# Kernel tuning notes

Hardware: AMD Instinct MI355X
Metric: run time of the kernel (lower is better)

Reference implementation:

```python
import jax, jax.numpy as jnp
import numpy as np

NUM_HEADS = 8
ALPHA = 4.0
BN_EPS = 1e-5


def _dwconv(x, w, pad):
    # x: [B, C, H, W], w: [C, 1, kh, kw] depthwise (groups == C)
    return jax.lax.conv_general_dilated(
        x, w, window_strides=(1, 1), padding=[(pad, pad), (pad, pad)],
        dimension_numbers=('NCHW', 'OIHW', 'NCHW'),
        feature_group_count=x.shape[1])


def _forward(x, qg_w, kv_w, proj_w, proj_b, dwc_w, dwc_b, power_p, scale_p,
             enh_w, bn_gamma, bn_beta, enhance_weight, pos_enc):
    B, N, C = x.shape
    H = W = int(round(N ** 0.5))
    h = NUM_HEADS
    d = C // h

    # qg linear (no bias): [B, N, 2C] -> q, g
    qg = jnp.einsum('bnc,oc->bno', x, qg_w)
    q, g = qg[..., :C], qg[..., C:]

    # SpatialFilterEnhancer on q: depthwise 3x3 conv + BN(train) + ReLU
    qi = q.transpose(0, 2, 1).reshape(B, C, H, W)
    qe = _dwconv(qi, enh_w, pad=1)
    m = qe.mean(axis=(0, 2, 3), keepdims=True)
    var = qe.var(axis=(0, 2, 3), keepdims=True)
    qe = (qe - m) * jax.lax.rsqrt(var + BN_EPS)
    qe = qe * bn_gamma[None, :, None, None] + bn_beta[None, :, None, None]
    qe = jax.nn.relu(qe)
    q_enh = qe.reshape(B, C, N).transpose(0, 2, 1)
    q = q + enhance_weight * q_enh

    # kv linear (sr_ratio == 1 path)
    kv = jnp.einsum('bnc,oc->bno', x, kv_w)
    k, v = kv[..., :C], kv[..., C:]
    k = k + pos_enc  # learned positional encoding, shape [1, N, C]
    n = k.shape[1]

    scale = jax.nn.softplus(scale_p)              # [1, 1, C]
    power = 1.0 + ALPHA * jax.nn.sigmoid(power_p)  # [1, h, 1, d]
    q = q / scale
    k = k / scale

    # split heads: [B, h, N, d]
    q = q.reshape(B, N, h, d).transpose(0, 2, 1, 3)
    k = k.reshape(B, n, h, d).transpose(0, 2, 1, 3)
    v = v.reshape(B, n, h, d).transpose(0, 2, 1, 3)

    # power-law kernel feature maps
    q_pos = jax.nn.relu(q) ** power
    q_neg = jax.nn.relu(-q) ** power
    k_pos = jax.nn.relu(k) ** power
    k_neg = jax.nn.relu(-k) ** power
    q_sim = jnp.concatenate([q_pos, q_neg], axis=-1)   # [B, h, N, 2d]
    q_opp = jnp.concatenate([q_neg, q_pos], axis=-1)
    kf = jnp.concatenate([k_pos, k_neg], axis=-1)      # [B, h, n, 2d]
    v1, v2 = jnp.split(v, 2, axis=-1)                  # [B, h, n, d/2] each

    k_mean = kf.mean(axis=-2)  # [B, h, 2d]
    inv_n = 1.0 / n

    # sim branch
    z = 1.0 / (jnp.einsum('bhnd,bhd->bhn', q_sim, k_mean)[..., None] + 1e-6)
    kv1 = jnp.einsum('bhnd,bhne->bhde', kf, v1) * inv_n  # (n^-0.5)*(n^-0.5)
    x_sim = jnp.einsum('bhnd,bhde->bhne', q_sim, kv1) * z

    # opp branch
    z2 = 1.0 / (jnp.einsum('bhnd,bhd->bhn', q_opp, k_mean)[..., None] + 1e-6)
    kv2 = jnp.einsum('bhnd,bhne->bhde', kf, v2) * inv_n
    x_opp = jnp.einsum('bhnd,bhde->bhne', q_opp, kv2) * z2

    xa = jnp.concatenate([x_sim, x_opp], axis=-1)       # [B, h, N, d]
    xa = xa.transpose(0, 2, 1, 3).reshape(B, N, C)

    # depthwise conv positional branch on v (sr_ratio == 1 -> no interpolate)
    vimg = v.reshape(B * h, H, W, d).transpose(0, 3, 1, 2)  # [B*h, d, H, W]
    vd = _dwconv(vimg, dwc_w, pad=2) + dwc_b[None, :, None, None]
    v_out = vd.reshape(B, C, N).transpose(0, 2, 1)          # [B, N, C]

    out = (xa + v_out) * g
    out = jnp.einsum('bnc,oc->bno', out, proj_w) + proj_b
    return out


def setup_inputs() -> dict:
    key = jax.random.key(0)
    ks = jax.random.split(key, 10)
    B, N, C = 8, 3136, 512
    h = NUM_HEADS
    d = C // h
    f = lambda k, shape, s=0.02: jax.random.normal(k, shape, jnp.float32) * s
    return dict(
        x=jax.random.normal(ks[0], (B, N, C), jnp.float32),
        qg_w=f(ks[1], (2 * C, C)),
        kv_w=f(ks[2], (2 * C, C)),
        proj_w=f(ks[3], (C, C)),
        proj_b=jnp.zeros((C,), jnp.float32),
        dwc_w=f(ks[4], (d, 1, 5, 5), 0.1),
        dwc_b=jnp.zeros((d,), jnp.float32),
        power_p=f(ks[5], (1, h, 1, d), 0.1),
        scale_p=f(ks[6], (1, 1, C), 0.1),
        enh_w=f(ks[7], (C, 1, 3, 3), 0.1),
        bn_gamma=jnp.ones((C,), jnp.float32),
        bn_beta=jnp.zeros((C,), jnp.float32),
        enhance_weight=jnp.float32(0.5),
        pos_enc=f(ks[8], (1, N, C)),
    )


def reference(x, qg_w, kv_w, proj_w, proj_b, dwc_w, dwc_b, power_p, scale_p,
              enh_w, bn_gamma, bn_beta, enhance_weight, pos_enc):
    return _forward(x, qg_w, kv_w, proj_w, proj_b, dwc_w, dwc_b, power_p,
                    scale_p, enh_w, bn_gamma, bn_beta, enhance_weight, pos_enc)
```

## Files before the change

### kernel.cpp

```cpp
#include <hip/hip_runtime.h>
#include <hip/hip_bf16.h>
#include <math.h>

#define CDIM 512
#define NTOK 3136
#define BATCH 8
#define MTOT (BATCH*NTOK)
#define NHEAD 8
#define DHEAD 64
#define HW 56

typedef __attribute__((ext_vector_type(8))) short short8;
typedef __attribute__((ext_vector_type(4))) float f32x4;

__device__ __forceinline__ ushort f2bf(float f) {
    union { float f; unsigned int u; } v; v.f = f;
    unsigned int u = v.u + 0x7FFFu + ((v.u >> 16) & 1u);
    return (ushort)(u >> 16);
}
__device__ __forceinline__ float bf2f(ushort u) {
    union { unsigned int u; float f; } v; v.u = ((unsigned int)u) << 16;
    return v.f;
}

__device__ __forceinline__ void gload_lds16(const void* g, void* lds) {
    __builtin_amdgcn_global_load_lds((const __attribute__((address_space(1))) void*)g,
                                     (__attribute__((address_space(3))) void*)lds,
                                     16, 0, 0);
}

__global__ __launch_bounds__(256) void cvt_bf16_kernel(const float* __restrict__ src,
                                                       ushort* __restrict__ dst, int n4) {
    int i = blockIdx.x * 256 + threadIdx.x;
    if (i < n4) {
        float4 f = ((const float4*)src)[i];
        ushort4 o;
        o.x = f2bf(f.x); o.y = f2bf(f.y); o.z = f2bf(f.z); o.w = f2bf(f.w);
        ((ushort4*)dst)[i] = o;
    }
}

__global__ __launch_bounds__(256) void cvt_weights_kernel(const float* __restrict__ qg_w,
                                                          const float* __restrict__ kv_w,
                                                          const float* __restrict__ proj_w,
                                                          ushort* __restrict__ Wqg,
                                                          ushort* __restrict__ Wkv,
                                                          ushort* __restrict__ Wproj,
                                                          const float* __restrict__ scale_p,
                                                          const float* __restrict__ power_p,
                                                          float* __restrict__ inv_scale,
                                                          float* __restrict__ power) {
    int blk = blockIdx.x;
    if (blk >= 1280) {
        int c = (blk - 1280) * 256 + threadIdx.x;
        float s = log1pf(expf(scale_p[c]));
        inv_scale[c] = 1.0f / s;
        power[c] = 1.0f + 4.0f / (1.0f + expf(-power_p[c]));
        return;
    }
    int i = blk * 256 + threadIdx.x;
    const float* src; ushort* dst; int idx;
    if (i < 131072)      { src = qg_w;   dst = Wqg;   idx = i; }
    else if (i < 262144) { src = kv_w;   dst = Wkv;   idx = i - 131072; }
    else                 { src = proj_w; dst = Wproj; idx = i - 262144; }
    float4 f = ((const float4*)src)[idx];
    ushort4 o;
    o.x = f2bf(f.x); o.y = f2bf(f.y); o.z = f2bf(f.z); o.w = f2bf(f.w);
    ((ushort4*)dst)[idx] = o;
}

__global__ __launch_bounds__(256, 3) void mgemm_qgkv(const ushort* __restrict__ A,
                                                     const ushort* __restrict__ Wqg,
                                                     const ushort* __restrict__ Wkv,
                                                     ushort* __restrict__ Qout,
                                                     ushort* __restrict__ Gout,
                                                     ushort* __restrict__ KFout,
                                                     ushort* __restrict__ Vout,
                                                     const float* __restrict__ pos,
                                                     const float* __restrict__ invs,
                                                     const float* __restrict__ powr) {
    __shared__ __align__(16) char smem[49152];
    ushort* At = (ushort*)smem;
    ushort* Bt = (ushort*)(smem + 24576);
    float*  Osh = (float*)smem;

    const int t = threadIdx.x;
    const int w = t >> 6, l = t & 63;
    const int wr = w >> 1, wc = w & 1;

    const int bid = blockIdx.x;
    const int idp = (bid & 7) * 392 + (bid >> 3);
    const int mb = idp >> 4, ob = idp & 15;
    const int m0 = mb * 128;
    const ushort* Bp = (ob < 8) ? (Wqg + (size_t)ob * 128 * CDIM)
                                : (Wkv + (size_t)(ob - 8) * 128 * CDIM);

    auto stage = [&](int buf, int ks) {
        const int k0 = ks * 32;
        #pragma unroll
        for (int i = 0; i < 2; ++i) {
            int f = t + i * 256;
            int row = f >> 2, ps = f & 3;
            int ls = ps ^ ((row >> 1) & 3);
            gload_lds16(A + (size_t)(m0 + row) * CDIM + k0 + ls * 8, At + buf * 4096 + f * 8);
            gload_lds16(Bp + (size_t)row * CDIM + k0 + ls * 8, Bt + buf * 4096 + f * 8);
        }
    };

    f32x4 acc[4][4] = {};
    stage(0, 0);
    stage(1, 1);
    const int sl4 = l >> 4;
    for (int ks = 0; ks < 16; ++ks) {
        if (ks < 15) asm volatile("s_waitcnt vmcnt(4)" ::: "memory");
        else         asm volatile("s_waitcnt vmcnt(0)" ::: "memory");
        __builtin_amdgcn_s_barrier();
        if (ks + 2 < 16) stage((ks + 2) % 3, ks + 2);
        const int cur = ks % 3;
        short8 af[4], bfr[4];
        #pragma unroll
        for (int i = 0; i < 4; ++i) {
            int row = wr * 64 + i * 16 + (l & 15);
            int ph = sl4 ^ ((row >> 1) & 3);
            af[i] = *(const short8*)&At[cur * 4096 + row * 32 + ph * 8];
            int rowb = wc * 64 + i * 16 + (l & 15);
            int phb = sl4 ^ ((rowb >> 1) & 3);
            bfr[i] = *(const short8*)&Bt[cur * 4096 + rowb * 32 + phb * 8];
        }
        #pragma unroll
        for (int i = 0; i < 4; ++i)
            #pragma unroll
            for (int j = 0; j < 4; ++j)
                acc[i][j] = __builtin_amdgcn_mfma_f32_16x16x32_bf16(af[i], bfr[j], acc[i][j], 0, 0, 0);
    }
    __syncthreads();

    const int colbase = ob * 128;
    #pragma unroll
    for (int p = 0; p < 2; ++p) {
        if (wr == p) {
            #pragma unroll
            for (int i = 0; i < 4; ++i)
                #pragma unroll
                for (int j = 0; j < 4; ++j)
                    #pragma unroll
                    for (int rr = 0; rr < 4; ++rr) {
                        int row = i * 16 + (l >> 4) * 4 + rr;
                        int col = wc * 64 + j * 16 + (l & 15);
                        int pc = col ^ (((row >> 2) & 1) << 4);
                        Osh[row * 128 + pc] = acc[i][j][rr];
                    }
        }
        __syncthreads();
        #pragma unroll
        for (int q = 0; q < 4; ++q) {
            int fi = q * 256 + t;
            int rl = fi >> 4;
            int c8 = (fi & 15) * 8;
            int xo = ((rl >> 2) & 1) << 4;
            float4 va = *(float4*)&Osh[rl * 128 + (c8 ^ xo)];
            float4 vb = *(float4*)&Osh[rl * 128 + ((c8 + 4) ^ xo)];
            int m = m0 + p * 64 + rl;
            if (colbase < 512) {
                union { ushort u[8]; short8 s; } o;
                o.u[0]=f2bf(va.x); o.u[1]=f2bf(va.y); o.u[2]=f2bf(va.z); o.u[3]=f2bf(va.w);
                o.u[4]=f2bf(vb.x); o.u[5]=f2bf(vb.y); o.u[6]=f2bf(vb.z); o.u[7]=f2bf(vb.w);
                *(short8*)&Qout[(size_t)m * CDIM + colbase + c8] = o.s;
            } else if (colbase < 1024) {
                union { ushort u[8]; short8 s; } o;
                o.u[0]=f2bf(va.x); o.u[1]=f2bf(va.y); o.u[2]=f2bf(va.z); o.u[3]=f2bf(va.w);
                o.u[4]=f2bf(vb.x); o.u[5]=f2bf(vb.y); o.u[6]=f2bf(vb.z); o.u[7]=f2bf(vb.w);
                *(short8*)&Gout[(size_t)m * CDIM + colbase - 512 + c8] = o.s;
            } else if (colbase < 1536) {
                int n = m % NTOK;
                int oc = colbase - 1024 + c8;
                const float* pp = &pos[(size_t)n * CDIM + oc];
                float4 pva = *(const float4*)pp;
                float4 pvb = *(const float4*)(pp + 4);
                float4 iva = *(const float4*)&invs[oc];
                float4 ivb = *(const float4*)&invs[oc + 4];
                float4 pwa = *(const float4*)&powr[oc];
                float4 pwb = *(const float4*)&powr[oc + 4];
                float kx[8], tp[8];
                kx[0]=(va.x+pva.x)*iva.x; kx[1]=(va.y+pva.y)*iva.y;
                kx[2]=(va.z+pva.z)*iva.z; kx[3]=(va.w+pva.w)*iva.w;
                kx[4]=(vb.x+pvb.x)*ivb.x; kx[5]=(vb.y+pvb.y)*ivb.y;
                kx[6]=(vb.z+pvb.z)*ivb.z; kx[7]=(vb.w+pvb.w)*ivb.w;
                tp[0]=__powf(fabsf(kx[0]),pwa.x); tp[1]=__powf(fabsf(kx[1]),pwa.y);
                tp[2]=__powf(fabsf(kx[2]),pwa.z); tp[3]=__powf(fabsf(kx[3]),pwa.w);
                tp[4]=__powf(fabsf(kx[4]),pwb.x); tp[5]=__powf(fabsf(kx[5]),pwb.y);
                tp[6]=__powf(fabsf(kx[6]),pwb.z); tp[7]=__powf(fabsf(kx[7]),pwb.w);
                union { ushort u[8]; short8 s; } up, un;
                #pragma unroll
                for (int e = 0; e < 8; ++e) {
                    ushort b = f2bf(tp[e]);
                    up.u[e] = kx[e] > 0.f ? b : (ushort)0;
                    un.u[e] = kx[e] < 0.f ? b : (ushort)0;
                }
                ushort* dst = KFout + (size_t)m * 1024 + ((oc >> 6) << 7) + (oc & 63);
                *(short8*)dst = up.s;
                *(short8*)(dst + 64) = un.s;
            } else {
                union { ushort u[8]; short8 s; } o;
                o.u[0]=f2bf(va.x); o.u[1]=f2bf(va.y); o.u[2]=f2bf(va.z); o.u[3]=f2bf(va.w);
                o.u[4]=f2bf(vb.x); o.u[5]=f2bf(vb.y); o.u[6]=f2bf(vb.z); o.u[7]=f2bf(vb.w);
                *(short8*)&Vout[(size_t)m * CDIM + colbase - 1536 + c8] = o.s;
            }
        }
        __syncthreads();
    }
}

__global__ __launch_bounds__(256) void mgemm_proj(const ushort* __restrict__ A,
                                                  const ushort* __restrict__ W,
                                                  float* __restrict__ out,
                                                  const float* __restrict__ pb) {
    __shared__ __align__(16) char smem[65536];
    ushort* At = (ushort*)smem;
    ushort* Bt = (ushort*)(smem + 32768);
    float*  Osh = (float*)smem;

    const int t = threadIdx.x;
    const int w = t >> 6, l = t & 63;
    const int wr = w >> 1, wc = w & 1;
    const int r8 = l >> 3, sl = l & 7;
    const int ss = sl ^ r8;

    const int bid = blockIdx.x;
    const int idp = (bid & 7) * 98 + (bid >> 3);
    const int mb = idp >> 2, ob = idp & 3;
    const int m0 = mb * 128;
    const ushort* Bp = W + (size_t)ob * 128 * CDIM;

    auto stage = [&](int buf, int ks) {
        const int k0 = ks * 64;
        #pragma unroll
        for (int c = 0; c < 4; ++c) {
            int rc = (w * 4 + c) * 8 + r8;
            gload_lds16(A + (size_t)(m0 + rc) * CDIM + k0 + ss * 8, At + buf * 8192 + (w * 4 + c) * 512);
            gload_lds16(Bp + (size_t)rc * CDIM + k0 + ss * 8, Bt + buf * 8192 + (w * 4 + c) * 512);
        }
    };

    f32x4 acc[4][4] = {};
    stage(0, 0);
    __syncthreads();
    for (int ks = 0; ks < 8; ++ks) {
        int cur = ks & 1;
        if (ks < 7) stage(cur ^ 1, ks + 1);
        #pragma unroll
        for (int kk = 0; kk < 2; ++kk) {
            short8 af[4], bfr[4];
            const int sbase = kk * 4 + (l >> 4);
            #pragma unroll
            for (int i = 0; i < 4; ++i) {
                int row = wr * 64 + i * 16 + (l & 15);
                af[i] = *(const short8*)&At[cur * 8192 + row * 64 + ((sbase ^ (row & 7)) * 8)];
                int rowb = wc * 64 + i * 16 + (l & 15);
                bfr[i] = *(const short8*)&Bt[cur * 8192 + rowb * 64 + ((sbase ^ (rowb & 7)) * 8)];
            }
            #pragma unroll
            for (int i = 0; i < 4; ++i)
                #pragma unroll
                for (int j = 0; j < 4; ++j)
                    acc[i][j] = __builtin_amdgcn_mfma_f32_16x16x32_bf16(af[i], bfr[j], acc[i][j], 0, 0, 0);
        }
        __syncthreads();
    }

    #pragma unroll
    for (int i = 0; i < 4; ++i)
        #pragma unroll
        for (int j = 0; j < 4; ++j)
            #pragma unroll
            for (int rr = 0; rr < 4; ++rr) {
                int row = wr * 64 + i * 16 + (l >> 4) * 4 + rr;
                int col = wc * 64 + j * 16 + (l & 15);
                int pc = col ^ (((row >> 2) & 1) << 4);
                Osh[row * 128 + pc] = acc[i][j][rr];
            }
    __syncthreads();

    const int colbase = ob * 128;
    #pragma unroll
    for (int q = 0; q < 16; ++q) {
        int fi = q * 256 + t;
        int r = fi >> 5, c4 = (fi & 31) * 4;
        int pc4 = c4 ^ (((r >> 2) & 1) << 4);
        float4 v = *(float4*)&Osh[r * 128 + pc4];
        float4 b4 = *(const float4*)&pb[colbase + c4];
        v.x += b4.x; v.y += b4.y; v.z += b4.z; v.w += b4.w;
        *(float4*)&out[(size_t)(m0 + r) * CDIM + colbase + c4] = v;
    }
}

__global__ __launch_bounds__(256) void conv3s_kernel(const ushort* __restrict__ Qbf,
                                                     const float* __restrict__ enh_w,
                                                     ushort* __restrict__ QEbf,
                                                     float* __restrict__ ssum,
                                                     float* __restrict__ ssq) {
    const int t = threadIdx.x;
    const int c0 = t * 2;
    const int xpos = blockIdx.x;
    const int byc = blockIdx.y;
    const int b = byc >> 2, yc = byc & 3;
    const int y0 = yc * 14;

    float wgt[9][2];
    #pragma unroll
    for (int tap = 0; tap < 9; ++tap) {
        wgt[tap][0] = enh_w[c0 * 9 + tap];
        wgt[tap][1] = enh_w[(c0 + 1) * 9 + tap];
    }
    const size_t base = (size_t)b * NTOK * CDIM + c0;

    float2 win[3][3];
    auto ldrow = [&](int yy, float2* dst) {
        #pragma unroll
        for (int dx = 0; dx < 3; ++dx) {
            int xx = xpos + dx - 1;
            bool ok = (yy >= 0 && yy < HW && xx >= 0 && xx < HW);
            if (ok) {
                ushort2 uv = *(const ushort2*)(Qbf + base + ((size_t)(yy * HW + xx) << 9));
                dst[dx] = make_float2(bf2f(uv.x), bf2f(uv.y));
            } else {
                dst[dx] = make_float2(0.f, 0.f);
            }
        }
    };
    ldrow(y0 - 1, win[0]);
    ldrow(y0,     win[1]);

    float s1a = 0.f, s2a = 0.f, s1b = 0.f, s2b = 0.f;
    #pragma unroll
    for (int i = 0; i < 14; ++i) {
        int y = y0 + i;
        ldrow(y + 1, win[(i + 2) % 3]);
        float a0 = 0.f, a1 = 0.f;
        #pragma unroll
        for (int dy = 0; dy < 3; ++dy) {
            float2* row = win[(i + dy) % 3];
            #pragma unroll
            for (int dx = 0; dx < 3; ++dx) {
                a0 = fmaf(row[dx].x, wgt[dy * 3 + dx][0], a0);
                a1 = fmaf(row[dx].y, wgt[dy * 3 + dx][1], a1);
            }
        }
        ushort2 o; o.x = f2bf(a0); o.y = f2bf(a1);
        *(ushort2*)(QEbf + base + ((size_t)(y * HW + xpos) << 9)) = o;
        s1a += a0; s2a += a0 * a0;
        s1b += a1; s2b += a1 * a1;
    }
    atomicAdd(&ssum[c0], s1a);     atomicAdd(&ssq[c0], s2a);
    atomicAdd(&ssum[c0 + 1], s1b); atomicAdd(&ssq[c0 + 1], s2b);
}

__global__ __launch_bounds__(256) void kvred4_kernel(const ushort* __restrict__ KF,
                                                     const ushort* __restrict__ Vbf,
                                                     float* __restrict__ PKV_A,
                                                     float* __restrict__ PKV_B) {
    const int bh = blockIdx.x, chunk = blockIdx.y;
    const int b = bh >> 3, head = bh & 7;
    const int t = threadIdx.x;
    const int w = t >> 6, l = t & 63;
    const int lr = l & 15;
    const int ns = (l >> 4) * 8;

    const int nbase = b * NTOK + chunk * 224;
    const ushort* kf0 = KF  + ((size_t)(nbase + ns)) * 1024 + head * 128 + (w * 32 + lr);
    const ushort* vb0 = Vbf + ((size_t)(nbase + ns)) * 512  + head * 64  + lr;

    short8 ones;
    #pragma unroll
    for (int j = 0; j < 8; ++j) ones[j] = (lr == 0) ? (short)0x3F80 : (short)0;

    f32x4 acc[2][5] = {};
    for (int tile = 0; tile < 7; ++tile) {
        union { uint u[4]; short8 s; } ua[2], ub[4];
        #pragma unroll
        for (int i = 0; i < 2; ++i) {
            #pragma unroll
            for (int j = 0; j < 4; ++j) {
                uint lo = kf0[i * 16 + (size_t)(2 * j) * 1024];
                uint hi = kf0[i * 16 + (size_t)(2 * j + 1) * 1024];
                ua[i].u[j] = lo | (hi << 16);
            }
        }
        #pragma unroll
        for (int j5 = 0; j5 < 4; ++j5) {
            #pragma unroll
            for (int j = 0; j < 4; ++j) {
                uint lo = vb0[j5 * 16 + (size_t)(2 * j) * 512];
                uint hi = vb0[j5 * 16 + (size_t)(2 * j + 1) * 512];
                ub[j5].u[j] = lo | (hi << 16);
            }
        }
        #pragma unroll
        for (int i = 0; i < 2; ++i) {
            #pragma unroll
            for (int j5 = 0; j5 < 4; ++j5)
                acc[i][j5] = __builtin_amdgcn_mfma_f32_16x16x32_bf16(ua[i].s, ub[j5].s, acc[i][j5], 0, 0, 0);
            acc[i][4] = __builtin_amdgcn_mfma_f32_16x16x32_bf16(ua[i].s, ones, acc[i][4], 0, 0, 0);
        }
        kf0 += (size_t)32 * 1024;
        vb0 += (size_t)32 * 512;
    }
    float* dstb = (chunk < 7)
        ? (PKV_A + ((size_t)(chunk * 64 + bh)) * 8320)
        : (PKV_B + ((size_t)((chunk - 7) * 64 + bh)) * 8320);
    #pragma unroll
    for (int i = 0; i < 2; ++i) {
        int d0 = w * 32 + i * 16 + (l >> 4) * 4;
        #pragma unroll
        for (int j = 0; j < 5; ++j) {
            int e = j * 16 + lr;
            if (j < 4 || e == 64)
                *(f32x4*)(dstb + (size_t)e * 128 + d0) = acc[i][j];
        }
    }
}

__global__ __launch_bounds__(256) void kvreduce2_kernel(const float* __restrict__ PKV_A,
                                                        const float* __restrict__ PKV_B,
                                                        ushort* __restrict__ kvTbf) {
    int gid = blockIdx.x * 256 + threadIdx.x;
    const float inv_n = 1.0f / (float)NTOK;
    int bh = gid / 10240;
    int r  = gid - bh * 10240;
    int row = r >> 7, dcol = r & 127;
    int dlog = (((dcol >> 3) ^ (row & 7)) << 3) | (dcol & 7);
    float s = 0.f;
    if (row < 66) {
        int rsel, dsel;
        if (row < 64) { rsel = row; dsel = (row >= 32) ? (dlog ^ 64) : dlog; }
        else          { rsel = 64;  dsel = (row == 65) ? (dlog ^ 64) : dlog; }
        size_t idx = (size_t)bh * 8320 + rsel * 128 + dsel;
        #pragma unroll
        for (int c = 0; c < 7; ++c) s += PKV_A[(size_t)c * 532480 + idx];
        #pragma unroll
        for (int c = 0; c < 7; ++c) s += PKV_B[(size_t)c * 532480 + idx];
    }
    kvTbf[gid] = (row < 66) ? f2bf(s * inv_n) : (ushort)0;
}

__global__ __launch_bounds__(256) void attn_mfma_kernel(const ushort* __restrict__ Qbf,
                                                        const ushort* __restrict__ QEbf,
                                                        const ushort* __restrict__ kvTbf,
                                                        const float* __restrict__ power,
                                                        const float* __restrict__ ssum,
                                                        const float* __restrict__ ssq,
                                                        const float* __restrict__ bn_g,
                                                        const float* __restrict__ bn_b,
                                                        const float* __restrict__ invs,
                                                        const float* __restrict__ ewp,
                                                        ushort* __restrict__ ATTbf) {
    __shared__ ushort QF[64 * 128];
    __shared__ ushort BT[80 * 128];
    const int bh = blockIdx.x, tb = blockIdx.y;
    const int b = bh >> 3, head = bh & 7;
    const int t = threadIdx.x;
    const int w = t >> 6, l = t & 63;

    #pragma unroll
    for (int i = 0; i < 5; ++i) {
        int f = i * 256 + t;
        gload_lds16(kvTbf + (size_t)bh * 10240 + f * 8, BT + f * 8);
    }

    const int c = l, hc = head * 64 + c;
    const float p = power[hc];
    const float invM = 1.0f / (float)MTOT;
    float mean = ssum[hc] * invM;
    float var  = ssq[hc] * invM - mean * mean;
    const float ac = bn_g[hc] * rsqrtf(var + 1e-5f);
    const float bc = bn_b[hc] - mean * ac;
    const float iv = invs[hc], ew = ewp[0];
    #pragma unroll
    for (int i = 0; i < 16; ++i) {
        int tok = i * 4 + w;
        size_t off = ((size_t)(b * NTOK + tb * 64 + tok)) * CDIM + hc;
        float q = bf2f(Qbf[off]);
        float qe = bf2f(QEbf[off]);
        q = (q + ew * fmaxf(fmaf(ac, qe, bc), 0.f)) * iv;
        float ax = fabsf(q);
        float tp = ax > 0.f ? __powf(ax, p) : 0.f;
        float qp = q > 0.f ? tp : 0.f;
        float qn = q < 0.f ? tp : 0.f;
        int sw = tok & 7;
        QF[tok * 128 + (((c >> 3) ^ sw) * 8) + (c & 7)]       = f2bf(qp);
        QF[tok * 128 + ((((c >> 3) + 8) ^ sw) * 8) + (c & 7)] = f2bf(qn);
    }
    __syncthreads();

    f32x4 acc[5] = {};
    #pragma unroll
    for (int kk = 0; kk < 4; ++kk) {
        int sbase = kk * 4 + (l >> 4);
        int rowa = w * 16 + (l & 15);
        short8 af = *(const short8*)&QF[rowa * 128 + ((sbase ^ (rowa & 7)) * 8)];
        #pragma unroll
        for (int j = 0; j < 5; ++j) {
            int rowb = j * 16 + (l & 15);
            short8 bf = *(const short8*)&BT[rowb * 128 + ((sbase ^ (rowb & 7)) * 8)];
            acc[j] = __builtin_amdgcn_mfma_f32_16x16x32_bf16(af, bf, acc[j], 0, 0, 0);
        }
    }
    __syncthreads();

    ushort* Oout = QF;
    #pragma unroll
    for (int rr = 0; rr < 4; ++rr) {
        float ssim = __shfl(acc[4][rr], (l & 48));
        float sopp = __shfl(acc[4][rr], (l & 48) + 1);
        float zs = 1.f / (ssim + 1e-6f);
        float zo = 1.f / (sopp + 1e-6f);
        int tokl = w * 16 + (l >> 4) * 4 + rr;
        #pragma unroll
        for (int j = 0; j < 4; ++j) {
            int e = j * 16 + (l & 15);
            Oout[tokl * 64 + e] = f2bf(acc[j][rr] * (j < 2 ? zs : zo));
        }
    }
    __syncthreads();

    #pragma unroll
    for (int i = 0; i < 2; ++i) {
        int idx = i * 256 + t;
        int tokl = idx >> 3, ch = (idx & 7) * 8;
        short8 vv = *(short8*)&Oout[tokl * 64 + ch];
        *(short8*)&ATTbf[((size_t)(b * NTOK + tb * 64 + tokl)) * CDIM + head * 64 + ch] = vv;
    }
}

__global__ __launch_bounds__(256) void voutg2_kernel(const ushort* __restrict__ Vbf,
                                                     const ushort* __restrict__ ATTbf,
                                                     const ushort* __restrict__ Gbf,
                                                     const float* __restrict__ dwc_w,
                                                     const float* __restrict__ dwc_b,
                                                     ushort* __restrict__ PRE) {
    const int t = threadIdx.x;
    const int c0 = t * 2;
    const int xpos = blockIdx.x;
    const int byc = blockIdx.y;
    const int b = byc >> 2, yc = byc & 3;
    const int y0 = yc * 14;
    const int dch = c0 & 63;

    float wgt[25][2];
    #pragma unroll
    for (int tap = 0; tap < 25; ++tap) {
        wgt[tap][0] = dwc_w[dch * 25 + tap];
        wgt[tap][1] = dwc_w[(dch + 1) * 25 + tap];
    }
    const float bias0 = dwc_b[dch], bias1 = dwc_b[dch + 1];
    const size_t base = (size_t)b * NTOK * CDIM + c0;

    float2 win[5][5];
    auto ldrow = [&](int yy, float2* dst) {
        #pragma unroll
        for (int dx = 0; dx < 5; ++dx) {
            int xx = xpos + dx - 2;
            bool ok = (yy >= 0 && yy < HW && xx >= 0 && xx < HW);
            if (ok) {
                ushort2 uv = *(const ushort2*)(Vbf + base + ((size_t)(yy * HW + xx) << 9));
                dst[dx] = make_float2(bf2f(uv.x), bf2f(uv.y));
            } else {
                dst[dx] = make_float2(0.f, 0.f);
            }
        }
    };
    ldrow(y0 - 2, win[0]);
    ldrow(y0 - 1, win[1]);
    ldrow(y0,     win[2]);
    ldrow(y0 + 1, win[3]);

    #pragma unroll
    for (int i = 0; i < 14; ++i) {
        int y = y0 + i;
        ldrow(y + 2, win[(i + 4) % 5]);
        float a0 = bias0, a1 = bias1;
        #pragma unroll
        for (int dy = 0; dy < 5; ++dy) {
            float2* row = win[(i + dy) % 5];
            #pragma unroll
            for (int dx = 0; dx < 5; ++dx) {
                a0 = fmaf(row[dx].x, wgt[dy * 5 + dx][0], a0);
                a1 = fmaf(row[dx].y, wgt[dy * 5 + dx][1], a1);
            }
        }
        size_t oidx = base + ((size_t)(y * HW + xpos) << 9);
        ushort2 au = *(const ushort2*)(ATTbf + oidx);
        ushort2 gu = *(const ushort2*)(Gbf + oidx);
        ushort2 o;
        o.x = f2bf((bf2f(au.x) + a0) * bf2f(gu.x));
        o.y = f2bf((bf2f(au.y) + a1) * bf2f(gu.y));
        *(ushort2*)(PRE + oidx) = o;
    }
}

extern "C" void kernel_launch(void* const* d_in, const int* in_sizes, int n_in,
                              void* d_out, int out_size, void* d_ws, size_t ws_size,
                              hipStream_t stream) {
    const float* x      = (const float*)d_in[0];
    const float* qg_w   = (const float*)d_in[1];
    const float* kv_w   = (const float*)d_in[2];
    const float* proj_w = (const float*)d_in[3];
    const float* proj_b = (const float*)d_in[4];
    const float* dwc_w  = (const float*)d_in[5];
    const float* dwc_b  = (const float*)d_in[6];
    const float* power_p= (const float*)d_in[7];
    const float* scale_p= (const float*)d_in[8];
    const float* enh_w  = (const float*)d_in[9];
    const float* bn_g   = (const float*)d_in[10];
    const float* bn_b   = (const float*)d_in[11];
    const float* ew_p   = (const float*)d_in[12];
    const float* pos    = (const float*)d_in[13];

    const size_t NELEM = (size_t)MTOT * CDIM;
    float* ws    = (float*)d_ws;
    ushort* Qbf  = (ushort*)ws;
    ushort* Gbf  = (ushort*)(ws + NELEM);
    float*  PKV_A= ws + NELEM + NELEM / 2;
    ushort* KFbf = (ushort*)(ws + 2 * NELEM);
    ushort* PREbf= (ushort*)(ws + 2 * NELEM);
    ushort* Vbf  = (ushort*)(ws + 3 * NELEM);
    ushort* ATTbf= (ushort*)(ws + 3 * NELEM + NELEM / 2);
    ushort* Xbf  = (ushort*)(ws + 4 * NELEM);
    ushort* QEbf = (ushort*)(ws + 4 * NELEM);
    float*  PKV_B= ws + 4 * NELEM + NELEM / 2;
    float* SMALL = ws + 5 * NELEM;
    float* ssum  = SMALL;
    float* ssq   = SMALL + 512;
    ushort* kvTbf= (ushort*)(SMALL + 9216);
    float* invs  = SMALL + 533504;
    float* powr  = SMALL + 534016;
    ushort* Wqg  = (ushort*)(SMALL + 535552);
    ushort* Wkv  = (ushort*)(SMALL + 797696);
    ushort* Wproj= (ushort*)(SMALL + 1059840);

    hipMemsetAsync(SMALL, 0, (size_t)1024 * sizeof(float), stream);

    cvt_bf16_kernel<<<12544, 256, 0, stream>>>(x, Xbf, 3211264);
    cvt_weights_kernel<<<1282, 256, 0, stream>>>(qg_w, kv_w, proj_w, Wqg, Wkv, Wproj,
                                                 scale_p, power_p, invs, powr);

    mgemm_qgkv<<<3136, 256, 0, stream>>>(Xbf, Wqg, Wkv, Qbf, Gbf, KFbf, Vbf, pos, invs, powr);

    dim3 cgrid(56, 32);
    conv3s_kernel<<<cgrid, 256, 0, stream>>>(Qbf, enh_w, QEbf, ssum, ssq);

    kvred4_kernel<<<dim3(64, 14), 256, 0, stream>>>(KFbf, Vbf, PKV_A, PKV_B);
    kvreduce2_kernel<<<2560, 256, 0, stream>>>(PKV_A, PKV_B, kvTbf);

    attn_mfma_kernel<<<dim3(64, 49), 256, 0, stream>>>(Qbf, QEbf, kvTbf, powr,
                                                       ssum, ssq, bn_g, bn_b,
                                                       invs, ew_p, ATTbf);

    voutg2_kernel<<<cgrid, 256, 0, stream>>>(Vbf, ATTbf, Gbf, dwc_w, dwc_b, PREbf);

    mgemm_proj<<<784, 256, 0, stream>>>(PREbf, Wproj, (float*)d_out, proj_b);
}
```

Before: 462.1 us.

## Merge conversion and mid-stage kernels; triple-buffer proj GEMM with smaller LDS

Folds the activation and weight bf16 conversions into one launch, and merges the depthwise-conv/BN-stats kernel with the KV reduction kernel into one launch using block-index dispatch, which removes launch gaps and lets the two independent stages run concurrently. The projection GEMM moves to K-steps of 32 with a 3-stage LDS ring, explicit vmcnt waits and barriers. It also writes the epilogue in two half passes so LDS drops to 48KB and 3 blocks per CU fit. This adds branch divergence at block granularity and more barriers in the GEMM loop.

```diff
diff --git a/kernel.cpp b/kernel.cpp
--- a/kernel.cpp
+++ b/kernel.cpp
@@ -29,36 +29,35 @@
                                      16, 0, 0);
 }
 
-__global__ __launch_bounds__(256) void cvt_bf16_kernel(const float* __restrict__ src,
-                                                       ushort* __restrict__ dst, int n4) {
-    int i = blockIdx.x * 256 + threadIdx.x;
-    if (i < n4) {
-        float4 f = ((const float4*)src)[i];
+__global__ __launch_bounds__(256) void cvt_all_kernel(const float* __restrict__ x,
+                                                      ushort* __restrict__ Xbf,
+                                                      const float* __restrict__ qg_w,
+                                                      const float* __restrict__ kv_w,
+                                                      const float* __restrict__ proj_w,
+                                                      ushort* __restrict__ Wqg,
+                                                      ushort* __restrict__ Wkv,
+                                                      ushort* __restrict__ Wproj,
+                                                      const float* __restrict__ scale_p,
+                                                      const float* __restrict__ power_p,
+                                                      float* __restrict__ inv_scale,
+                                                      float* __restrict__ power) {
+    int blk = blockIdx.x;
+    if (blk < 12544) {
+        int i = blk * 256 + threadIdx.x;
+        float4 f = ((const float4*)x)[i];
         ushort4 o;
         o.x = f2bf(f.x); o.y = f2bf(f.y); o.z = f2bf(f.z); o.w = f2bf(f.w);
-        ((ushort4*)dst)[i] = o;
-    }
-}
-
-__global__ __launch_bounds__(256) void cvt_weights_kernel(const float* __restrict__ qg_w,
-                                                          const float* __restrict__ kv_w,
-                                                          const float* __restrict__ proj_w,
-                                                          ushort* __restrict__ Wqg,
-                                                          ushort* __restrict__ Wkv,
-                                                          ushort* __restrict__ Wproj,
-                                                          const float* __restrict__ scale_p,
-                                                          const float* __restrict__ power_p,
-                                                          float* __restrict__ inv_scale,
-                                                          float* __restrict__ power) {
-    int blk = blockIdx.x;
-    if (blk >= 1280) {
-        int c = (blk - 1280) * 256 + threadIdx.x;
+        ((ushort4*)Xbf)[i] = o;
+        return;
+    }
+    if (blk >= 13824) {
+        int c = (blk - 13824) * 256 + threadIdx.x;
         float s = log1pf(expf(scale_p[c]));
         inv_scale[c] = 1.0f / s;
         power[c] = 1.0f + 4.0f / (1.0f + expf(-power_p[c]));
         return;
     }
-    int i = blk * 256 + threadIdx.x;
+    int i = (blk - 12544) * 256 + threadIdx.x;
     const float* src; ushort* dst; int idx;
     if (i < 131072)      { src = qg_w;   dst = Wqg;   idx = i; }
     else if (i < 262144) { src = kv_w;   dst = Wkv;   idx = i - 131072; }
@@ -193,9 +192,9 @@
                 union { ushort u[8]; short8 s; } up, un;
                 #pragma unroll
                 for (int e = 0; e < 8; ++e) {
-                    ushort b = f2bf(tp[e]);
-                    up.u[e] = kx[e] > 0.f ? b : (ushort)0;
-                    un.u[e] = kx[e] < 0.f ? b : (ushort)0;
+                    ushort bb = f2bf(tp[e]);
+                    up.u[e] = kx[e] > 0.f ? bb : (ushort)0;
+                    un.u[e] = kx[e] < 0.f ? bb : (ushort)0;
                 }
                 ushort* dst = KFout + (size_t)m * 1024 + ((oc >> 6) << 7) + (oc & 63);
                 *(short8*)dst = up.s;
@@ -211,20 +210,18 @@
     }
 }
 
-__global__ __launch_bounds__(256) void mgemm_proj(const ushort* __restrict__ A,
-                                                  const ushort* __restrict__ W,
-                                                  float* __restrict__ out,
-                                                  const float* __restrict__ pb) {
-    __shared__ __align__(16) char smem[65536];
+__global__ __launch_bounds__(256, 3) void mgemm_proj(const ushort* __restrict__ A,
+                                                     const ushort* __restrict__ W,
+                                                     float* __restrict__ out,
+                                                     const float* __restrict__ pb) {
+    __shared__ __align__(16) char smem[49152];
     ushort* At = (ushort*)smem;
-    ushort* Bt = (ushort*)(smem + 32768);
+    ushort* Bt = (ushort*)(smem + 24576);
     float*  Osh = (float*)smem;
 
     const int t = threadIdx.x;
     const int w = t >> 6, l = t & 63;
     const int wr = w >> 1, wc = w & 1;
-    const int r8 = l >> 3, sl = l & 7;
-    const int ss = sl ^ r8;
 
     const int bid = blockIdx.x;
     const int idp = (bid & 7) * 98 + (bid >> 3);
@@ -233,190 +230,203 @@
     const ushort* Bp = W + (size_t)ob * 128 * CDIM;
 
     auto stage = [&](int buf, int ks) {
-        const int k0 = ks * 64;
-        #pragma unroll
-        for (int c = 0; c < 4; ++c) {
-            int rc = (w * 4 + c) * 8 + r8;
-            gload_lds16(A + (size_t)(m0 + rc) * CDIM + k0 + ss * 8, At + buf * 8192 + (w * 4 + c) * 512);
-            gload_lds16(Bp + (size_t)rc * CDIM + k0 + ss * 8, Bt + buf * 8192 + (w * 4 + c) * 512);
+        const int k0 = ks * 32;
+        #pragma unroll
+        for (int i = 0; i < 2; ++i) {
+            int f = t + i * 256;
+            int row = f >> 2, ps = f & 3;
+            int ls = ps ^ ((row >> 1) & 3);
+            gload_lds16(A + (size_t)(m0 + row) * CDIM + k0 + ls * 8, At + buf * 4096 + f * 8);
+            gload_lds16(Bp + (size_t)row * CDIM + k0 + ls * 8, Bt + buf * 4096 + f * 8);
         }
     };
 
     f32x4 acc[4][4] = {};
     stage(0, 0);
+    stage(1, 1);
+    const int sl4 = l >> 4;
+    for (int ks = 0; ks < 16; ++ks) {
+        if (ks < 15) asm volatile("s_waitcnt vmcnt(4)" ::: "memory");
+        else         asm volatile("s_waitcnt vmcnt(0)" ::: "memory");
+        __builtin_amdgcn_s_barrier();
+        if (ks + 2 < 16) stage((ks + 2) % 3, ks + 2);
+        const int cur = ks % 3;
+        short8 af[4], bfr[4];
+        #pragma unroll
+        for (int i = 0; i < 4; ++i) {
+            int row = wr * 64 + i * 16 + (l & 15);
+            int ph = sl4 ^ ((row >> 1) & 3);
+            af[i] = *(const short8*)&At[cur * 4096 + row * 32 + ph * 8];
+            int rowb = wc * 64 + i * 16 + (l & 15);
+            int phb = sl4 ^ ((rowb >> 1) & 3);
+            bfr[i] = *(const short8*)&Bt[cur * 4096 + rowb * 32 + phb * 8];
+        }
+        #pragma unroll
+        for (int i = 0; i < 4; ++i)
+            #pragma unroll
+            for (int j = 0; j < 4; ++j)
+                acc[i][j] = __builtin_amdgcn_mfma_f32_16x16x32_bf16(af[i], bfr[j], acc[i][j], 0, 0, 0);
+    }
     __syncthreads();
-    for (int ks = 0; ks < 8; ++ks) {
-        int cur = ks & 1;
-        if (ks < 7) stage(cur ^ 1, ks + 1);
-        #pragma unroll
-        for (int kk = 0; kk < 2; ++kk) {
-            short8 af[4], bfr[4];
-            const int sbase = kk * 4 + (l >> 4);
-            #pragma unroll
-            for (int i = 0; i < 4; ++i) {
-                int row = wr * 64 + i * 16 + (l & 15);
-                af[i] = *(const short8*)&At[cur * 8192 + row * 64 + ((sbase ^ (row & 7)) * 8)];
-                int rowb = wc * 64 + i * 16 + (l & 15);
-                bfr[i] = *(const short8*)&Bt[cur * 8192 + rowb * 64 + ((sbase ^ (rowb & 7)) * 8)];
-            }
+
+    const int colbase = ob * 128;
+    #pragma unroll
+    for (int p = 0; p < 2; ++p) {
+        if (wr == p) {
             #pragma unroll
             for (int i = 0; i < 4; ++i)
                 #pragma unroll
                 for (int j = 0; j < 4; ++j)
-                    acc[i][j] = __builtin_amdgcn_mfma_f32_16x16x32_bf16(af[i], bfr[j], acc[i][j], 0, 0, 0);
+                    #pragma unroll
+                    for (int rr = 0; rr < 4; ++rr) {
+                        int row = i * 16 + (l >> 4) * 4 + rr;
+                        int col = wc * 64 + j * 16 + (l & 15);
+                        int pc = col ^ (((row >> 2) & 1) << 4);
+                        Osh[row * 128 + pc] = acc[i][j][rr];
+                    }
         }
         __syncthreads();
-    }
-
-    #pragma unroll
-    for (int i = 0; i < 4; ++i)
-        #pragma unroll
-        for (int j = 0; j < 4; ++j)
-            #pragma unroll
-            for (int rr = 0; rr < 4; ++rr) {
-                int row = wr * 64 + i * 16 + (l >> 4) * 4 + rr;
-                int col = wc * 64 + j * 16 + (l & 15);
-                int pc = col ^ (((row >> 2) & 1) << 4);
-                Osh[row * 128 + pc] = acc[i][j][rr];
-            }
-    __syncthreads();
-
-    const int colbase = ob * 128;
-    #pragma unroll
-    for (int q = 0; q < 16; ++q) {
-        int fi = q * 256 + t;
-        int r = fi >> 5, c4 = (fi & 31) * 4;
-        int pc4 = c4 ^ (((r >> 2) & 1) << 4);
-        float4 v = *(float4*)&Osh[r * 128 + pc4];
-        float4 b4 = *(const float4*)&pb[colbase + c4];
-        v.x += b4.x; v.y += b4.y; v.z += b4.z; v.w += b4.w;
-        *(float4*)&out[(size_t)(m0 + r) * CDIM + colbase + c4] = v;
-    }
-}
-
-__global__ __launch_bounds__(256) void conv3s_kernel(const ushort* __restrict__ Qbf,
-                                                     const float* __restrict__ enh_w,
-                                                     ushort* __restrict__ QEbf,
-                                                     float* __restrict__ ssum,
-                                                     float* __restrict__ ssq) {
+        #pragma unroll
+        for (int q = 0; q < 8; ++q) {
+            int fi = q * 256 + t;
+            int rl = fi >> 5, c4 = (fi & 31) * 4;
+            int pc4 = c4 ^ (((rl >> 2) & 1) << 4);
+            float4 v = *(float4*)&Osh[rl * 128 + pc4];
+            float4 b4 = *(const float4*)&pb[colbase + c4];
+            v.x += b4.x; v.y += b4.y; v.z += b4.z; v.w += b4.w;
+            *(float4*)&out[(size_t)(m0 + p * 64 + rl) * CDIM + colbase + c4] = v;
+        }
+        __syncthreads();
+    }
+}
+
+__global__ __launch_bounds__(256) void fused_mid_kernel(const ushort* __restrict__ KF,
+                                                        const ushort* __restrict__ Vbf,
+                                                        float* __restrict__ PKV_A,
+                                                        float* __restrict__ PKV_B,
+                                                        const ushort* __restrict__ Qbf,
+                                                        const float* __restrict__ enh_w,
+                                                        ushort* __restrict__ QEbf,
+                                                        float* __restrict__ ssum,
+                                                        float* __restrict__ ssq) {
+    const int blk = blockIdx.x;
     const int t = threadIdx.x;
-    const int c0 = t * 2;
-    const int xpos = blockIdx.x;
-    const int byc = blockIdx.y;
-    const int b = byc >> 2, yc = byc & 3;
-    const int y0 = yc * 14;
-
-    float wgt[9][2];
-    #pragma unroll
-    for (int tap = 0; tap < 9; ++tap) {
-        wgt[tap][0] = enh_w[c0 * 9 + tap];
-        wgt[tap][1] = enh_w[(c0 + 1) * 9 + tap];
-    }
-    const size_t base = (size_t)b * NTOK * CDIM + c0;
-
-    float2 win[3][3];
-    auto ldrow = [&](int yy, float2* dst) {
-        #pragma unroll
-        for (int dx = 0; dx < 3; ++dx) {
-            int xx = xpos + dx - 1;
-            bool ok = (yy >= 0 && yy < HW && xx >= 0 && xx < HW);
-            if (ok) {
-                ushort2 uv = *(const ushort2*)(Qbf + base + ((size_t)(yy * HW + xx) << 9));
-                dst[dx] = make_float2(bf2f(uv.x), bf2f(uv.y));
-            } else {
-                dst[dx] = make_float2(0.f, 0.f);
-            }
-        }
-    };
-    ldrow(y0 - 1, win[0]);
-    ldrow(y0,     win[1]);
-
-    float s1a = 0.f, s2a = 0.f, s1b = 0.f, s2b = 0.f;
-    #pragma unroll
-    for (int i = 0; i < 14; ++i) {
-        int y = y0 + i;
-        ldrow(y + 1, win[(i + 2) % 3]);
-        float a0 = 0.f, a1 = 0.f;
-        #pragma unroll
-        for (int dy = 0; dy < 3; ++dy) {
-            float2* row = win[(i + dy) % 3];
+    if (blk < 896) {
+        const int bh = blk & 63, chunk = blk >> 6;
+        const int b = bh >> 3, head = bh & 7;
+        const int w = t >> 6, l = t & 63;
+        const int lr = l & 15;
+        const int ns = (l >> 4) * 8;
+
+        const int nbase = b * NTOK + chunk * 224;
+        const ushort* kf0 = KF  + ((size_t)(nbase + ns)) * 1024 + head * 128 + (w * 32 + lr);
+        const ushort* vb0 = Vbf + ((size_t)(nbase + ns)) * 512  + head * 64  + lr;
+
+        short8 ones;
+        #pragma unroll
+        for (int j = 0; j < 8; ++j) ones[j] = (lr == 0) ? (short)0x3F80 : (short)0;
+
+        f32x4 acc[2][5] = {};
+        for (int tile = 0; tile < 7; ++tile) {
+            union { uint u[4]; short8 s; } ua[2], ub[4];
+            #pragma unroll
+            for (int i = 0; i < 2; ++i) {
+                #pragma unroll
+                for (int j = 0; j < 4; ++j) {
+                    uint lo = kf0[i * 16 + (size_t)(2 * j) * 1024];
+                    uint hi = kf0[i * 16 + (size_t)(2 * j + 1) * 1024];
+                    ua[i].u[j] = lo | (hi << 16);
+                }
+            }
+            #pragma unroll
+            for (int j5 = 0; j5 < 4; ++j5) {
+                #pragma unroll
+                for (int j = 0; j < 4; ++j) {
+                    uint lo = vb0[j5 * 16 + (size_t)(2 * j) * 512];
+                    uint hi = vb0[j5 * 16 + (size_t)(2 * j + 1) * 512];
+                    ub[j5].u[j] = lo | (hi << 16);
+                }
+            }
+            #pragma unroll
+            for (int i = 0; i < 2; ++i) {
+                #pragma unroll
+                for (int j5 = 0; j5 < 4; ++j5)
+                    acc[i][j5] = __builtin_amdgcn_mfma_f32_16x16x32_bf16(ua[i].s, ub[j5].s, acc[i][j5], 0, 0, 0);
+                acc[i][4] = __builtin_amdgcn_mfma_f32_16x16x32_bf16(ua[i].s, ones, acc[i][4], 0, 0, 0);
+            }
+            kf0 += (size_t)32 * 1024;
+            vb0 += (size_t)32 * 512;
+        }
+        float* dstb = (chunk < 7)
+            ? (PKV_A + ((size_t)(chunk * 64 + bh)) * 8320)
+            : (PKV_B + ((size_t)((chunk - 7) * 64 + bh)) * 8320);
+        #pragma unroll
+        for (int i = 0; i < 2; ++i) {
+            int d0 = w * 32 + i * 16 + (l >> 4) * 4;
+            #pragma unroll
+            for (int j = 0; j < 5; ++j) {
+                int e = j * 16 + lr;
+                if (j < 4 || e == 64)
+                    *(f32x4*)(dstb + (size_t)e * 128 + d0) = acc[i][j];
+            }
+        }
+        return;
+    }
+    {
+        const int idx = blk - 896;
+        const int xpos = idx % 56;
+        const int byc = idx / 56;
+        const int c0 = t * 2;
+        const int b = byc >> 2, yc = byc & 3;
+        const int y0 = yc * 14;
+
+        float wgt[9][2];
+        #pragma unroll
+        for (int tap = 0; tap < 9; ++tap) {
+            wgt[tap][0] = enh_w[c0 * 9 + tap];
+            wgt[tap][1] = enh_w[(c0 + 1) * 9 + tap];
+        }
+        const size_t base = (size_t)b * NTOK * CDIM + c0;
+
+        float2 win[3][3];
+        auto ldrow = [&](int yy, float2* dst) {
             #pragma unroll
             for (int dx = 0; dx < 3; ++dx) {
-                a0 = fmaf(row[dx].x, wgt[dy * 3 + dx][0], a0);
-                a1 = fmaf(row[dx].y, wgt[dy * 3 + dx][1], a1);
-            }
-        }
-        ushort2 o; o.x = f2bf(a0); o.y = f2bf(a1);
-        *(ushort2*)(QEbf + base + ((size_t)(y * HW + xpos) << 9)) = o;
-        s1a += a0; s2a += a0 * a0;
-        s1b += a1; s2b += a1 * a1;
-    }
-    atomicAdd(&ssum[c0], s1a);     atomicAdd(&ssq[c0], s2a);
-    atomicAdd(&ssum[c0 + 1], s1b); atomicAdd(&ssq[c0 + 1], s2b);
-}
-
-__global__ __launch_bounds__(256) void kvred4_kernel(const ushort* __restrict__ KF,
-                                                     const ushort* __restrict__ Vbf,
-                                                     float* __restrict__ PKV_A,
-                                                     float* __restrict__ PKV_B) {
-    const int bh = blockIdx.x, chunk = blockIdx.y;
-    const int b = bh >> 3, head = bh & 7;
-    const int t = threadIdx.x;
-    const int w = t >> 6, l = t & 63;
-    const int lr = l & 15;
-    const int ns = (l >> 4) * 8;
-
-    const int nbase = b * NTOK + chunk * 224;
-    const ushort* kf0 = KF  + ((size_t)(nbase + ns)) * 1024 + head * 128 + (w * 32 + lr);
-    const ushort* vb0 = Vbf + ((size_t)(nbase + ns)) * 512  + head * 64  + lr;
-
-    short8 ones;
-    #pragma unroll
-    for (int j = 0; j < 8; ++j) ones[j] = (lr == 0) ? (short)0x3F80 : (short)0;
-
-    f32x4 acc[2][5] = {};
-    for (int tile = 0; tile < 7; ++tile) {
-        union { uint u[4]; short8 s; } ua[2], ub[4];
-        #pragma unroll
-        for (int i = 0; i < 2; ++i) {
-            #pragma unroll
-            for (int j = 0; j < 4; ++j) {
-                uint lo = kf0[i * 16 + (size_t)(2 * j) * 1024];
-                uint hi = kf0[i * 16 + (size_t)(2 * j + 1) * 1024];
-                ua[i].u[j] = lo | (hi << 16);
-            }
-        }
-        #pragma unroll
-        for (int j5 = 0; j5 < 4; ++j5) {
-            #pragma unroll
-            for (int j = 0; j < 4; ++j) {
-                uint lo = vb0[j5 * 16 + (size_t)(2 * j) * 512];
-                uint hi = vb0[j5 * 16 + (size_t)(2 * j + 1) * 512];
-                ub[j5].u[j] = lo | (hi << 16);
-            }
-        }
-        #pragma unroll
-        for (int i = 0; i < 2; ++i) {
-            #pragma unroll
-            for (int j5 = 0; j5 < 4; ++j5)
-                acc[i][j5] = __builtin_amdgcn_mfma_f32_16x16x32_bf16(ua[i].s, ub[j5].s, acc[i][j5], 0, 0, 0);
-            acc[i][4] = __builtin_amdgcn_mfma_f32_16x16x32_bf16(ua[i].s, ones, acc[i][4], 0, 0, 0);
-        }
-        kf0 += (size_t)32 * 1024;
-        vb0 += (size_t)32 * 512;
-    }
-    float* dstb = (chunk < 7)
-        ? (PKV_A + ((size_t)(chunk * 64 + bh)) * 8320)
-        : (PKV_B + ((size_t)((chunk - 7) * 64 + bh)) * 8320);
-    #pragma unroll
-    for (int i = 0; i < 2; ++i) {
-        int d0 = w * 32 + i * 16 + (l >> 4) * 4;
-        #pragma unroll
-        for (int j = 0; j < 5; ++j) {
-            int e = j * 16 + lr;
-            if (j < 4 || e == 64)
-                *(f32x4*)(dstb + (size_t)e * 128 + d0) = acc[i][j];
-        }
+                int xx = xpos + dx - 1;
+                bool ok = (yy >= 0 && yy < HW && xx >= 0 && xx < HW);
+                if (ok) {
+                    ushort2 uv = *(const ushort2*)(Qbf + base + ((size_t)(yy * HW + xx) << 9));
+                    dst[dx] = make_float2(bf2f(uv.x), bf2f(uv.y));
+                } else {
+                    dst[dx] = make_float2(0.f, 0.f);
+                }
+            }
+        };
+        ldrow(y0 - 1, win[0]);
+        ldrow(y0,     win[1]);
+
+        float s1a = 0.f, s2a = 0.f, s1b = 0.f, s2b = 0.f;
+        #pragma unroll
+        for (int i = 0; i < 14; ++i) {
+            int y = y0 + i;
+            ldrow(y + 1, win[(i + 2) % 3]);
+            float a0 = 0.f, a1 = 0.f;
+            #pragma unroll
+            for (int dy = 0; dy < 3; ++dy) {
+                float2* row = win[(i + dy) % 3];
+                #pragma unroll
+                for (int dx = 0; dx < 3; ++dx) {
+                    a0 = fmaf(row[dx].x, wgt[dy * 3 + dx][0], a0);
+                    a1 = fmaf(row[dx].y, wgt[dy * 3 + dx][1], a1);
+                }
+            }
+            ushort2 o; o.x = f2bf(a0); o.y = f2bf(a1);
+            *(ushort2*)(QEbf + base + ((size_t)(y * HW + xpos) << 9)) = o;
+            s1a += a0; s2a += a0 * a0;
+            s1b += a1; s2b += a1 * a1;
+        }
+        atomicAdd(&ssum[c0], s1a);     atomicAdd(&ssq[c0], s2a);
+        atomicAdd(&ssum[c0 + 1], s1b); atomicAdd(&ssq[c0 + 1], s2b);
     }
 }
 
@@ -640,23 +650,22 @@
 
     hipMemsetAsync(SMALL, 0, (size_t)1024 * sizeof(float), stream);
 
-    cvt_bf16_kernel<<<12544, 256, 0, stream>>>(x, Xbf, 3211264);
-    cvt_weights_kernel<<<1282, 256, 0, stream>>>(qg_w, kv_w, proj_w, Wqg, Wkv, Wproj,
-                                                 scale_p, power_p, invs, powr);
+    cvt_all_kernel<<<13826, 256, 0, stream>>>(x, Xbf, qg_w, kv_w, proj_w,
+                                              Wqg, Wkv, Wproj,
+                                              scale_p, power_p, invs, powr);
 
     mgemm_qgkv<<<3136, 256, 0, stream>>>(Xbf, Wqg, Wkv, Qbf, Gbf, KFbf, Vbf, pos, invs, powr);
 
-    dim3 cgrid(56, 32);
-    conv3s_kernel<<<cgrid, 256, 0, stream>>>(Qbf, enh_w, QEbf, ssum, ssq);
-
-    kvred4_kernel<<<dim3(64, 14), 256, 0, stream>>>(KFbf, Vbf, PKV_A, PKV_B);
+    fused_mid_kernel<<<2688, 256, 0, stream>>>(KFbf, Vbf, PKV_A, PKV_B,
+                                               Qbf, enh_w, QEbf, ssum, ssq);
+
     kvreduce2_kernel<<<2560, 256, 0, stream>>>(PKV_A, PKV_B, kvTbf);
 
     attn_mfma_kernel<<<dim3(64, 49), 256, 0, stream>>>(Qbf, QEbf, kvTbf, powr,
                                                        ssum, ssq, bn_g, bn_b,
                                                        invs, ew_p, ATTbf);
 
-    voutg2_kernel<<<cgrid, 256, 0, stream>>>(Vbf, ATTbf, Gbf, dwc_w, dwc_b, PREbf);
+    voutg2_kernel<<<dim3(56, 32), 256, 0, stream>>>(Vbf, ATTbf, Gbf, dwc_w, dwc_b, PREbf);
 
     mgemm_proj<<<784, 256, 0, stream>>>(PREbf, Wproj, (float*)d_out, proj_b);
 }
```

Result: faster. 448.5 us (median of 2 runs) (-2.9%).
